# Kernel tuning notes

Hardware: AMD Instinct MI355X
Metric: run time of the kernel (lower is better)

The kernel has to match this reference:

```python
import jax, jax.numpy as jnp
import numpy as np

N = 50000      # nodes
E = 800000     # edges (avg degree 16)
F_IN = 64      # node_feature_space
H = 64         # hidden_dim
G = 16         # graphs in batch
BN_EPS = 1e-5


def setup_inputs() -> dict:
    key = jax.random.key(0)
    ks = jax.random.split(key, 8)
    x = jax.random.normal(ks[0], (N, F_IN), jnp.float32)
    edge_index = jax.random.randint(ks[1], (2, E), 0, N, dtype=jnp.int64)
    batch = jnp.sort(jax.random.randint(ks[2], (N,), 0, G, dtype=jnp.int64))
    init = lambda k, shp, fan: jax.random.normal(k, shp, jnp.float32) / np.float32(np.sqrt(fan))
    params = dict(
        W1_0=init(ks[3], (F_IN, H), F_IN), b1_0=jnp.zeros((H,), jnp.float32),
        W2_0=init(ks[4], (H, H), H),       b2_0=jnp.zeros((H,), jnp.float32),
        g_0=jnp.ones((H,), jnp.float32),   be_0=jnp.zeros((H,), jnp.float32),
        W1_1=init(ks[5], (H, H), H),       b1_1=jnp.zeros((H,), jnp.float32),
        W2_1=init(ks[6], (H, H), H),       b2_1=jnp.zeros((H,), jnp.float32),
        g_1=jnp.ones((H,), jnp.float32),   be_1=jnp.zeros((H,), jnp.float32),
    )
    return dict(x=x, edge_index=edge_index, batch=batch, **params)


def _gin_layer(x, src, dst, W1, b1, W2, b2, g, be):
    # GINConv (eps=0): h_i = MLP(x_i + sum_{j->i} x_j)
    agg = jax.ops.segment_sum(x[src], dst, num_segments=N)   # [N, d]
    h = x + agg
    h = jnp.maximum(h @ W1 + b1, 0.0) @ W2 + b2              # Linear-ReLU-Linear
    # BatchNorm1d (training-mode batch stats, biased variance as in torch)
    mu = h.mean(axis=0)
    var = h.var(axis=0)
    h = (h - mu) * jax.lax.rsqrt(var + BN_EPS) * g + be
    return jnp.maximum(h, 0.0)                               # ReLU


def reference(x, edge_index, batch,
              W1_0, b1_0, W2_0, b2_0, g_0, be_0,
              W1_1, b1_1, W2_1, b2_1, g_1, be_1):
    src, dst = edge_index[0], edge_index[1]
    x = _gin_layer(x, src, dst, W1_0, b1_0, W2_0, b2_0, g_0, be_0)
    x = _gin_layer(x, src, dst, W1_1, b1_1, W2_1, b2_1, g_1, be_1)
    # global_mean_pool over graph ids
    cnt = jax.ops.segment_sum(jnp.ones((N,), x.dtype), batch, num_segments=G)
    sums = jax.ops.segment_sum(x, batch, num_segments=G)
    h_graph = sums / jnp.maximum(cnt, 1.0)[:, None]
    return (x, h_graph)
```

## Files before the change

### kernel.cpp

```cpp
#include <hip/hip_runtime.h>
#include <hip/hip_bf16.h>


constexpr int NN = 50000;
constexpr int NE = 800000;
constexpr int HD = 64;
constexpr int NG = 16;
constexpr float BN_EPS = 1e-5f;
constexpr int SCAN_BLOCKS = (NN + 255) / 256;
constexpr int NBUCK = (NN + 1023) / 1024;
constexpr int BIN1_BLOCKS = (NE + 4095) / 4096;

__global__ __launch_bounds__(256)
void x2bf_kernel(const float* __restrict__ x, __hip_bfloat16* __restrict__ xb,
                 int* __restrict__ cnt) {
    int i4 = blockIdx.x * 256 + threadIdx.x;
    if (i4 < NN) cnt[i4] = 0;
    if (i4 >= NN * HD / 4) return;
    float4 v = *(const float4*)(x + (size_t)i4 * 4);
    union { ushort4 u; __hip_bfloat16 b[4]; } p;
    p.b[0] = __float2bfloat16(v.x);
    p.b[1] = __float2bfloat16(v.y);
    p.b[2] = __float2bfloat16(v.z);
    p.b[3] = __float2bfloat16(v.w);
    *(ushort4*)((unsigned short*)xb + (size_t)i4 * 4) = p.u;
}

__global__ __launch_bounds__(256)
void count_kernel(const int* __restrict__ ei, int* __restrict__ cnt) {
    int e4 = (blockIdx.x * 256 + threadIdx.x) * 4;
    if (e4 >= NE) return;
    int4 d = *(const int4*)(ei + NE + e4);
    atomicAdd(&cnt[d.x], 1);
    atomicAdd(&cnt[d.y], 1);
    atomicAdd(&cnt[d.z], 1);
    atomicAdd(&cnt[d.w], 1);
}

__global__ __launch_bounds__(256)
void scan1_kernel(const int* __restrict__ cnt, int* __restrict__ row_ptr,
                  int* __restrict__ partials) {
    int i = blockIdx.x * 256 + threadIdx.x;
    int v = (i < NN) ? cnt[i] : 0;
    __shared__ int s[256];
    s[threadIdx.x] = v;
    __syncthreads();
#pragma unroll
    for (int off = 1; off < 256; off <<= 1) {
        int add = (threadIdx.x >= off) ? s[threadIdx.x - off] : 0;
        __syncthreads();
        s[threadIdx.x] += add;
        __syncthreads();
    }
    if (i < NN) row_ptr[i] = s[threadIdx.x] - v;
    if (threadIdx.x == 255) partials[blockIdx.x] = s[255];
}

__global__ __launch_bounds__(256)
void scan3_kernel(int* __restrict__ row_ptr, const int* __restrict__ partials,
                  int* __restrict__ gcur) {
    __shared__ int s[256];
    __shared__ int orig[256];
    int v = (threadIdx.x < SCAN_BLOCKS) ? partials[threadIdx.x] : 0;
    s[threadIdx.x] = v;
    orig[threadIdx.x] = v;
    __syncthreads();
#pragma unroll
    for (int off = 1; off < 256; off <<= 1) {
        int add = (threadIdx.x >= off) ? s[threadIdx.x - off] : 0;
        __syncthreads();
        s[threadIdx.x] += add;
        __syncthreads();
    }
    int poff = s[blockIdx.x] - orig[blockIdx.x];
    int i = blockIdx.x * 256 + threadIdx.x;
    if (i < NN) {
        int rv = row_ptr[i] + poff;
        row_ptr[i] = rv;
        if ((i & 1023) == 0) gcur[i >> 10] = rv;
    }
    if (i == 0) row_ptr[NN] = NE;
}

__global__ __launch_bounds__(256)
void bin1_kernel(const int* __restrict__ ei, int* __restrict__ gcur,
                 int2* __restrict__ part) {
    __shared__ int lcnt[NBUCK];
    __shared__ int lbase[NBUCK];
    __shared__ int lcur[NBUCK];
    int tid = threadIdx.x;
    int chunk = blockIdx.x * 4096;
    if (tid < NBUCK) lcnt[tid] = 0;
    __syncthreads();
#pragma unroll
    for (int r = 0; r < 16; r++) {
        int e = chunk + r * 256 + tid;
        if (e < NE) atomicAdd(&lcnt[ei[NE + e] >> 10], 1);
    }
    __syncthreads();
    if (tid < NBUCK) {
        lbase[tid] = atomicAdd(&gcur[tid], lcnt[tid]);
        lcur[tid] = 0;
    }
    __syncthreads();
#pragma unroll
    for (int r = 0; r < 16; r++) {
        int e = chunk + r * 256 + tid;
        if (e < NE) {
            int src = ei[e];
            int dst = ei[NE + e];
            int b = dst >> 10;
            int slot = atomicAdd(&lcur[b], 1);
            part[lbase[b] + slot] = make_int2(src, dst);
        }
    }
}

__global__ __launch_bounds__(256)
void bin2_kernel(const int2* __restrict__ part, const int* __restrict__ row_ptr,
                 int* __restrict__ csr) {
    __shared__ int lcur[1024];
    int b = blockIdx.x;
    int base_row = b << 10;
    for (int i = threadIdx.x; i < 1024; i += 256)
        lcur[i] = row_ptr[min(base_row + i, NN)];
    __syncthreads();
    int s = row_ptr[min(base_row, NN)];
    int e = row_ptr[min(base_row + 1024, NN)];
    for (int i = s + threadIdx.x; i < e; i += 256) {
        int2 p = part[i];
        int pos = atomicAdd(&lcur[p.y & 1023], 1);
        csr[pos] = p.x;
    }
}

__global__ __launch_bounds__(256)
void agg_kernel(const float* __restrict__ x, const __hip_bfloat16* __restrict__ xb,
                const int* __restrict__ row_ptr, const int* __restrict__ csr,
                float* __restrict__ h, float* __restrict__ stats) {
    if (blockIdx.x == 0 && threadIdx.x < 128) stats[threadIdx.x] = 0.f;
    int row = blockIdx.x * 4 + (threadIdx.x >> 6);
    int lane = threadIdx.x & 63;
    int s = row_ptr[row], e = row_ptr[row + 1];
    int cnt = e - s;
    int ids = (lane < cnt) ? csr[s + lane] : 0;
    float acc = x[(size_t)row * HD + lane];
    int m = min(cnt, 64);
    int j = 0;
    float a0 = 0.f, a1 = 0.f, a2 = 0.f, a3 = 0.f;
    float a4 = 0.f, a5 = 0.f, a6 = 0.f, a7 = 0.f;
    for (; j + 8 <= m; j += 8) {
        int nb0 = __shfl(ids, j);
        int nb1 = __shfl(ids, j + 1);
        int nb2 = __shfl(ids, j + 2);
        int nb3 = __shfl(ids, j + 3);
        int nb4 = __shfl(ids, j + 4);
        int nb5 = __shfl(ids, j + 5);
        int nb6 = __shfl(ids, j + 6);
        int nb7 = __shfl(ids, j + 7);
        a0 += __bfloat162float(xb[(size_t)nb0 * HD + lane]);
        a1 += __bfloat162float(xb[(size_t)nb1 * HD + lane]);
        a2 += __bfloat162float(xb[(size_t)nb2 * HD + lane]);
        a3 += __bfloat162float(xb[(size_t)nb3 * HD + lane]);
        a4 += __bfloat162float(xb[(size_t)nb4 * HD + lane]);
        a5 += __bfloat162float(xb[(size_t)nb5 * HD + lane]);
        a6 += __bfloat162float(xb[(size_t)nb6 * HD + lane]);
        a7 += __bfloat162float(xb[(size_t)nb7 * HD + lane]);
    }
    acc += ((a0 + a1) + (a2 + a3)) + ((a4 + a5) + (a6 + a7));
    for (; j < m; j++) {
        int nb = __shfl(ids, j);
        acc += __bfloat162float(xb[(size_t)nb * HD + lane]);
    }
    for (int jj = s + 64; jj < e; jj++) {
        acc += __bfloat162float(xb[(size_t)csr[jj] * HD + lane]);
    }
    h[(size_t)row * HD + lane] = acc;
}

__global__ __launch_bounds__(256)
void aggn_kernel(const float* __restrict__ hraw, const __hip_bfloat16* __restrict__ xbr,
                 const int* __restrict__ row_ptr, const int* __restrict__ csr,
                 const float* __restrict__ stats_prev, const float* __restrict__ g0,
                 const float* __restrict__ be0,
                 float* __restrict__ h, float* __restrict__ stats_next) {
    if (blockIdx.x == 0 && threadIdx.x < 128) stats_next[threadIdx.x] = 0.f;
    int row = blockIdx.x * 4 + (threadIdx.x >> 6);
    int lane = threadIdx.x & 63;
    const float inv = 1.f / (float)NN;
    float mu = stats_prev[lane] * inv;
    float var = stats_prev[64 + lane] * inv - mu * mu;
    float sc = g0[lane] * rsqrtf(var + BN_EPS);
    float off = be0[lane] - mu * sc;
    int s = row_ptr[row], e = row_ptr[row + 1];
    int cnt = e - s;
    int ids = (lane < cnt) ? csr[s + lane] : 0;
    float acc = fmaxf(fmaf(hraw[(size_t)row * HD + lane], sc, off), 0.f);
    int m = min(cnt, 64);
    int j = 0;
    float a0 = 0.f, a1 = 0.f, a2 = 0.f, a3 = 0.f;
    float a4 = 0.f, a5 = 0.f, a6 = 0.f, a7 = 0.f;
    for (; j + 8 <= m; j += 8) {
        int nb0 = __shfl(ids, j);
        int nb1 = __shfl(ids, j + 1);
        int nb2 = __shfl(ids, j + 2);
        int nb3 = __shfl(ids, j + 3);
        int nb4 = __shfl(ids, j + 4);
        int nb5 = __shfl(ids, j + 5);
        int nb6 = __shfl(ids, j + 6);
        int nb7 = __shfl(ids, j + 7);
        float v0 = __bfloat162float(xbr[(size_t)nb0 * HD + lane]);
        float v1 = __bfloat162float(xbr[(size_t)nb1 * HD + lane]);
        float v2 = __bfloat162float(xbr[(size_t)nb2 * HD + lane]);
        float v3 = __bfloat162float(xbr[(size_t)nb3 * HD + lane]);
        float v4 = __bfloat162float(xbr[(size_t)nb4 * HD + lane]);
        float v5 = __bfloat162float(xbr[(size_t)nb5 * HD + lane]);
        float v6 = __bfloat162float(xbr[(size_t)nb6 * HD + lane]);
        float v7 = __bfloat162float(xbr[(size_t)nb7 * HD + lane]);
        a0 += fmaxf(fmaf(v0, sc, off), 0.f);
        a1 += fmaxf(fmaf(v1, sc, off), 0.f);
        a2 += fmaxf(fmaf(v2, sc, off), 0.f);
        a3 += fmaxf(fmaf(v3, sc, off), 0.f);
        a4 += fmaxf(fmaf(v4, sc, off), 0.f);
        a5 += fmaxf(fmaf(v5, sc, off), 0.f);
        a6 += fmaxf(fmaf(v6, sc, off), 0.f);
        a7 += fmaxf(fmaf(v7, sc, off), 0.f);
    }
    acc += ((a0 + a1) + (a2 + a3)) + ((a4 + a5) + (a6 + a7));
    for (; j < m; j++) {
        int nb = __shfl(ids, j);
        float v = __bfloat162float(xbr[(size_t)nb * HD + lane]);
        acc += fmaxf(fmaf(v, sc, off), 0.f);
    }
    for (int jj = s + 64; jj < e; jj++) {
        float v = __bfloat162float(xbr[(size_t)csr[jj] * HD + lane]);
        acc += fmaxf(fmaf(v, sc, off), 0.f);
    }
    h[(size_t)row * HD + lane] = acc;
}

__global__ __launch_bounds__(256)
void mlp_kernel(const float* __restrict__ hin, float* __restrict__ hout,
                const float* __restrict__ W1, const float* __restrict__ b1,
                const float* __restrict__ W2, const float* __restrict__ b2,
                float* __restrict__ stats, float* __restrict__ psums,
                __hip_bfloat16* __restrict__ xbr) {
    __shared__ float sh[128 * 65];
    __shared__ float sW[64 * 64];
    __shared__ float sb[64];
    __shared__ float red[2][4][64];
    int tid = threadIdx.x;
    int base = blockIdx.x * 128;

    if (blockIdx.x == 0) {
        float4 z = make_float4(0.f, 0.f, 0.f, 0.f);
        *(float4*)(psums + tid * 4) = z;
    }
    for (int i = tid; i < 4096; i += 256) sW[i] = W1[i];
    if (tid < 64) sb[tid] = b1[tid];
#pragma unroll
    for (int i = 0; i < 8; i++) {
        int i4 = tid + 256 * i;
        int row = i4 >> 4, col = (i4 & 15) * 4;
        int grow = base + row;
        float4 v = (grow < NN) ? *(const float4*)(hin + (size_t)grow * HD + col)
                               : make_float4(0.f, 0.f, 0.f, 0.f);
        float* d = sh + row * 65 + col;
        d[0] = v.x; d[1] = v.y; d[2] = v.z; d[3] = v.w;
    }
    __syncthreads();

    int wv = tid >> 6;
    int lane = tid & 63;

    float acc0[16], acc1[16];
#pragma unroll
    for (int j = 0; j < 16; j++) { acc0[j] = sb[wv * 16 + j]; acc1[j] = acc0[j]; }
    for (int k = 0; k < 64; k++) {
        float a0 = sh[lane * 65 + k];
        float a1 = sh[(64 + lane) * 65 + k];
        const float4* wr = (const float4*)(sW + k * 64 + wv * 16);
#pragma unroll
        for (int q = 0; q < 4; q++) {
            float4 w = wr[q];
            acc0[4 * q + 0] = fmaf(a0, w.x, acc0[4 * q + 0]);
            acc0[4 * q + 1] = fmaf(a0, w.y, acc0[4 * q + 1]);
            acc0[4 * q + 2] = fmaf(a0, w.z, acc0[4 * q + 2]);
            acc0[4 * q + 3] = fmaf(a0, w.w, acc0[4 * q + 3]);
            acc1[4 * q + 0] = fmaf(a1, w.x, acc1[4 * q + 0]);
            acc1[4 * q + 1] = fmaf(a1, w.y, acc1[4 * q + 1]);
            acc1[4 * q + 2] = fmaf(a1, w.z, acc1[4 * q + 2]);
            acc1[4 * q + 3] = fmaf(a1, w.w, acc1[4 * q + 3]);
        }
    }
    __syncthreads();

#pragma unroll
    for (int j = 0; j < 16; j++) {
        sh[lane * 65 + wv * 16 + j] = fmaxf(acc0[j], 0.f);
        sh[(64 + lane) * 65 + wv * 16 + j] = fmaxf(acc1[j], 0.f);
    }
    for (int i = tid; i < 4096; i += 256) sW[i] = W2[i];
    if (tid < 64) sb[tid] = b2[tid];
    __syncthreads();

#pragma unroll
    for (int j = 0; j < 16; j++) { acc0[j] = sb[wv * 16 + j]; acc1[j] = acc0[j]; }
    for (int k = 0; k < 64; k++) {
        float a0 = sh[lane * 65 + k];
        float a1 = sh[(64 + lane) * 65 + k];
        const float4* wr = (const float4*)(sW + k * 64 + wv * 16);
#pragma unroll
        for (int q = 0; q < 4; q++) {
            float4 w = wr[q];
            acc0[4 * q + 0] = fmaf(a0, w.x, acc0[4 * q + 0]);
            acc0[4 * q + 1] = fmaf(a0, w.y, acc0[4 * q + 1]);
            acc0[4 * q + 2] = fmaf(a0, w.z, acc0[4 * q + 2]);
            acc0[4 * q + 3] = fmaf(a0, w.w, acc0[4 * q + 3]);
            acc1[4 * q + 0] = fmaf(a1, w.x, acc1[4 * q + 0]);
            acc1[4 * q + 1] = fmaf(a1, w.y, acc1[4 * q + 1]);
            acc1[4 * q + 2] = fmaf(a1, w.z, acc1[4 * q + 2]);
            acc1[4 * q + 3] = fmaf(a1, w.w, acc1[4 * q + 3]);
        }
    }
    __syncthreads();
#pragma unroll
    for (int j = 0; j < 16; j++) {
        sh[lane * 65 + wv * 16 + j] = acc0[j];
        sh[(64 + lane) * 65 + wv * 16 + j] = acc1[j];
    }
    __syncthreads();

#pragma unroll
    for (int i = 0; i < 8; i++) {
        int i4 = tid + 256 * i;
        int row = i4 >> 4, col = (i4 & 15) * 4;
        int grow = base + row;
        if (grow < NN) {
            const float* s = sh + row * 65 + col;
            float4 v = make_float4(s[0], s[1], s[2], s[3]);
            *(float4*)(hout + (size_t)grow * HD + col) = v;
            if (xbr) {
                union { ushort4 u; __hip_bfloat16 b[4]; } p;
                p.b[0] = __float2bfloat16(v.x);
                p.b[1] = __float2bfloat16(v.y);
                p.b[2] = __float2bfloat16(v.z);
                p.b[3] = __float2bfloat16(v.w);
                *(ushort4*)((unsigned short*)xbr + (size_t)grow * HD + col) = p.u;
            }
        }
    }

    {
        int col = tid & 63;
        int r0 = (tid >> 6) * 32;
        float s = 0.f, ss = 0.f;
#pragma unroll
        for (int r = 0; r < 32; r++) {
            float v = (base + r0 + r < NN) ? sh[(r0 + r) * 65 + col] : 0.f;
            s += v;
            ss += v * v;
        }
        red[0][tid >> 6][col] = s;
        red[1][tid >> 6][col] = ss;
        __syncthreads();
        if (tid < 64) {
            float S = red[0][0][col] + red[0][1][col] + red[0][2][col] + red[0][3][col];
            atomicAdd(stats + col, S);
        } else if (tid < 128) {
            float SS = red[1][0][col] + red[1][1][col] + red[1][2][col] + red[1][3][col];
            atomicAdd(stats + 64 + col, SS);
        }
    }
}

__global__ __launch_bounds__(256)
void norm_kernel(float* h, const float* __restrict__ stats,
                 const float* __restrict__ g, const float* __restrict__ be,
                 const int* __restrict__ batch, float* __restrict__ psums) {
    __shared__ float sg[2][64];
    if (threadIdx.x < 128) sg[threadIdx.x >> 6][threadIdx.x & 63] = 0.f;
    __syncthreads();
    size_t i4 = (size_t)blockIdx.x * 256 + threadIdx.x;
    int row = (int)(i4 >> 4);
    int base_row = blockIdx.x * 16;
    int g0 = batch[base_row];
    size_t off = i4 * 4;
    int col = (int)(off & 63);
    float4 v = *(const float4*)(h + off);
    float4 sm = *(const float4*)(stats + col);
    float4 sq = *(const float4*)(stats + 64 + col);
    float4 gg = *(const float4*)(g + col);
    float4 bb = *(const float4*)(be + col);
    const float inv = 1.f / (float)NN;
    float4 o;
    {
        float mu = sm.x * inv, var = sq.x * inv - mu * mu;
        float sc = gg.x * rsqrtf(var + BN_EPS);
        o.x = fmaxf((v.x - mu) * sc + bb.x, 0.f);
    }
    {
        float mu = sm.y * inv, var = sq.y * inv - mu * mu;
        float sc = gg.y * rsqrtf(var + BN_EPS);
        o.y = fmaxf((v.y - mu) * sc + bb.y, 0.f);
    }
    {
        float mu = sm.z * inv, var = sq.z * inv - mu * mu;
        float sc = gg.z * rsqrtf(var + BN_EPS);
        o.z = fmaxf((v.z - mu) * sc + bb.z, 0.f);
    }
    {
        float mu = sm.w * inv, var = sq.w * inv - mu * mu;
        float sc = gg.w * rsqrtf(var + BN_EPS);
        o.w = fmaxf((v.w - mu) * sc + bb.w, 0.f);
    }
    *(float4*)(h + off) = o;

    int dg = batch[row] - g0;
    if (dg <= 1) {
        atomicAdd(&sg[dg][col + 0], o.x);
        atomicAdd(&sg[dg][col + 1], o.y);
        atomicAdd(&sg[dg][col + 2], o.z);
        atomicAdd(&sg[dg][col + 3], o.w);
    } else {
        int gid = g0 + dg;
        atomicAdd(&psums[gid * HD + col + 0], o.x);
        atomicAdd(&psums[gid * HD + col + 1], o.y);
        atomicAdd(&psums[gid * HD + col + 2], o.z);
        atomicAdd(&psums[gid * HD + col + 3], o.w);
    }
    __syncthreads();
    if (threadIdx.x < 128) {
        int d = threadIdx.x >> 6;
        int c = threadIdx.x & 63;
        float s = sg[d][c];
        if (g0 + d < NG && s != 0.f) atomicAdd(&psums[(g0 + d) * HD + c], s);
    }
}

__device__ __forceinline__ int lower_bound_batch(const int* __restrict__ b, int val) {
    int lo = 0, hi = NN;
    while (lo < hi) {
        int mid = (lo + hi) >> 1;
        if (b[mid] < val) lo = mid + 1;
        else hi = mid;
    }
    return lo;
}

__global__ __launch_bounds__(1024)
void pool_finalize_kernel(const float* __restrict__ sums, const int* __restrict__ batch,
                          float* __restrict__ out) {
    int g = threadIdx.x >> 6;
    int col = threadIdx.x & 63;
    int s = lower_bound_batch(batch, g);
    int e = lower_bound_batch(batch, g + 1);
    float cnt = (float)(e - s);
    out[g * HD + col] = sums[g * HD + col] / fmaxf(cnt, 1.f);
}

extern "C" void kernel_launch(void* const* d_in, const int* in_sizes, int n_in,
                              void* d_out, int out_size, void* d_ws, size_t ws_size,
                              hipStream_t stream) {
    const float* x = (const float*)d_in[0];
    const int* ei = (const int*)d_in[1];
    const int* batch = (const int*)d_in[2];
    const float* W1_0 = (const float*)d_in[3];
    const float* b1_0 = (const float*)d_in[4];
    const float* W2_0 = (const float*)d_in[5];
    const float* b2_0 = (const float*)d_in[6];
    const float* g_0 = (const float*)d_in[7];
    const float* be_0 = (const float*)d_in[8];
    const float* W1_1 = (const float*)d_in[9];
    const float* b1_1 = (const float*)d_in[10];
    const float* W2_1 = (const float*)d_in[11];
    const float* b2_1 = (const float*)d_in[12];
    const float* g_1 = (const float*)d_in[13];
    const float* be_1 = (const float*)d_in[14];

    float* out = (float*)d_out;

    float* buf_h = (float*)d_ws;
    float* stats0 = buf_h + (size_t)NN * HD;
    float* stats1 = stats0 + 128;
    float* psums = stats1 + 128;
    int* row_ptr = (int*)(psums + 1024);
    int* cnt = row_ptr + (NN + 2);
    int* partials = cnt + NN;
    int* gcur = partials + 256;
    int* csr = gcur + 64;
    __hip_bfloat16* xb = (__hip_bfloat16*)(csr + NE);
    int2* part = (int2*)(xb + (size_t)NN * HD);

    dim3 b256(256);
    int mlp_grid = (NN + 127) / 128;
    int norm_grid = (NN * HD / 4 + 255) / 256;
    int cnt_grid = (NE / 4 + 255) / 256;
    int agg_grid = NN / 4;

    x2bf_kernel<<<norm_grid, b256, 0, stream>>>(x, xb, cnt);
    count_kernel<<<cnt_grid, b256, 0, stream>>>(ei, cnt);
    scan1_kernel<<<SCAN_BLOCKS, b256, 0, stream>>>(cnt, row_ptr, partials);
    scan3_kernel<<<SCAN_BLOCKS, b256, 0, stream>>>(row_ptr, partials, gcur);
    bin1_kernel<<<BIN1_BLOCKS, b256, 0, stream>>>(ei, gcur, part);
    bin2_kernel<<<NBUCK, b256, 0, stream>>>(part, row_ptr, csr);

    agg_kernel<<<agg_grid, b256, 0, stream>>>(x, xb, row_ptr, csr, buf_h, stats0);
    mlp_kernel<<<mlp_grid, b256, 0, stream>>>(buf_h, out, W1_0, b1_0, W2_0, b2_0,
                                              stats0, psums, xb);

    aggn_kernel<<<agg_grid, b256, 0, stream>>>(out, xb, row_ptr, csr,
                                               stats0, g_0, be_0, buf_h, stats1);
    mlp_kernel<<<mlp_grid, b256, 0, stream>>>(buf_h, out, W1_1, b1_1, W2_1, b2_1,
                                              stats1, psums, (__hip_bfloat16*)nullptr);

    norm_kernel<<<norm_grid, b256, 0, stream>>>(out, stats1, g_1, be_1, batch, psums);
    pool_finalize_kernel<<<1, dim3(1024), 0, stream>>>(psums, batch, out + (size_t)NN * HD);
}
```

Before: 322.2 us.

## Merge scan passes with decoupled lookback and fold pooling finalize into norm

```diff
diff --git a/kernel.cpp b/kernel.cpp
--- a/kernel.cpp
+++ b/kernel.cpp
@@ -13,9 +13,10 @@
 
 __global__ __launch_bounds__(256)
 void x2bf_kernel(const float* __restrict__ x, __hip_bfloat16* __restrict__ xb,
-                 int* __restrict__ cnt) {
+                 int* __restrict__ cnt, int* __restrict__ flags) {
     int i4 = blockIdx.x * 256 + threadIdx.x;
     if (i4 < NN) cnt[i4] = 0;
+    if (i4 < 256) flags[i4] = 0;
     if (i4 >= NN * HD / 4) return;
     float4 v = *(const float4*)(x + (size_t)i4 * 4);
     union { ushort4 u; __hip_bfloat16 b[4]; } p;
@@ -38,11 +39,13 @@
 }
 
 __global__ __launch_bounds__(256)
-void scan1_kernel(const int* __restrict__ cnt, int* __restrict__ row_ptr,
-                  int* __restrict__ partials) {
-    int i = blockIdx.x * 256 + threadIdx.x;
+void scan_kernel(const int* __restrict__ cnt, int* __restrict__ row_ptr,
+                 int* __restrict__ flags, int* __restrict__ gcur) {
+    int b = blockIdx.x;
+    int i = b * 256 + threadIdx.x;
     int v = (i < NN) ? cnt[i] : 0;
     __shared__ int s[256];
+    __shared__ int pre[256];
     s[threadIdx.x] = v;
     __syncthreads();
 #pragma unroll
@@ -52,30 +55,23 @@
         s[threadIdx.x] += add;
         __syncthreads();
     }
-    if (i < NN) row_ptr[i] = s[threadIdx.x] - v;
-    if (threadIdx.x == 255) partials[blockIdx.x] = s[255];
-}
-
-__global__ __launch_bounds__(256)
-void scan3_kernel(int* __restrict__ row_ptr, const int* __restrict__ partials,
-                  int* __restrict__ gcur) {
-    __shared__ int s[256];
-    __shared__ int orig[256];
-    int v = (threadIdx.x < SCAN_BLOCKS) ? partials[threadIdx.x] : 0;
-    s[threadIdx.x] = v;
-    orig[threadIdx.x] = v;
-    __syncthreads();
-#pragma unroll
-    for (int off = 1; off < 256; off <<= 1) {
-        int add = (threadIdx.x >= off) ? s[threadIdx.x - off] : 0;
+    if (threadIdx.x == 255) atomicExch(&flags[b], s[255] | 0x40000000);
+    int pv = 0;
+    if (threadIdx.x < b) {
+        int f;
+        do { f = atomicAdd(&flags[threadIdx.x], 0); } while (f == 0);
+        pv = f & 0x3FFFFFFF;
+    }
+    pre[threadIdx.x] = pv;
+    __syncthreads();
+#pragma unroll
+    for (int off = 128; off > 0; off >>= 1) {
+        if (threadIdx.x < off) pre[threadIdx.x] += pre[threadIdx.x + off];
         __syncthreads();
-        s[threadIdx.x] += add;
-        __syncthreads();
-    }
-    int poff = s[blockIdx.x] - orig[blockIdx.x];
-    int i = blockIdx.x * 256 + threadIdx.x;
+    }
+    int poff = pre[0];
     if (i < NN) {
-        int rv = row_ptr[i] + poff;
+        int rv = s[threadIdx.x] - v + poff;
         row_ptr[i] = rv;
         if ((i & 1023) == 0) gcur[i >> 10] = rv;
     }
@@ -243,7 +239,7 @@
 void mlp_kernel(const float* __restrict__ hin, float* __restrict__ hout,
                 const float* __restrict__ W1, const float* __restrict__ b1,
                 const float* __restrict__ W2, const float* __restrict__ b2,
-                float* __restrict__ stats, float* __restrict__ psums,
+                float* __restrict__ stats, float* __restrict__ gout,
                 __hip_bfloat16* __restrict__ xbr) {
     __shared__ float sh[128 * 65];
     __shared__ float sW[64 * 64];
@@ -254,7 +250,7 @@
 
     if (blockIdx.x == 0) {
         float4 z = make_float4(0.f, 0.f, 0.f, 0.f);
-        *(float4*)(psums + tid * 4) = z;
+        *(float4*)(gout + tid * 4) = z;
     }
     for (int i = tid; i < 4096; i += 256) sW[i] = W1[i];
     if (tid < 64) sb[tid] = b1[tid];
@@ -374,17 +370,40 @@
     }
 }
 
+__device__ __forceinline__ int lower_bound_batch(const int* __restrict__ b, int val) {
+    int lo = 0, hi = NN;
+    while (lo < hi) {
+        int mid = (lo + hi) >> 1;
+        if (b[mid] < val) lo = mid + 1;
+        else hi = mid;
+    }
+    return lo;
+}
+
 __global__ __launch_bounds__(256)
 void norm_kernel(float* h, const float* __restrict__ stats,
                  const float* __restrict__ g, const float* __restrict__ be,
-                 const int* __restrict__ batch, float* __restrict__ psums) {
+                 const int* __restrict__ batch, float* __restrict__ gout) {
     __shared__ float sg[2][64];
-    if (threadIdx.x < 128) sg[threadIdx.x >> 6][threadIdx.x & 63] = 0.f;
-    __syncthreads();
-    size_t i4 = (size_t)blockIdx.x * 256 + threadIdx.x;
-    int row = (int)(i4 >> 4);
+    __shared__ float rinv[2];
+    int tid = threadIdx.x;
+    if (tid < 128) sg[tid >> 6][tid & 63] = 0.f;
     int base_row = blockIdx.x * 16;
     int g0 = batch[base_row];
+    if (tid < 2) {
+        int gg = g0 + tid;
+        float r = 0.f;
+        if (gg < NG) {
+            int s = lower_bound_batch(batch, gg);
+            int e = lower_bound_batch(batch, gg + 1);
+            r = 1.f / fmaxf((float)(e - s), 1.f);
+        }
+        rinv[tid] = r;
+    }
+    __syncthreads();
+
+    size_t i4 = (size_t)blockIdx.x * 256 + tid;
+    int row = (int)(i4 >> 4);
     size_t off = i4 * 4;
     int col = (int)(off & 63);
     float4 v = *(const float4*)(h + off);
@@ -424,39 +443,22 @@
         atomicAdd(&sg[dg][col + 3], o.w);
     } else {
         int gid = g0 + dg;
-        atomicAdd(&psums[gid * HD + col + 0], o.x);
-        atomicAdd(&psums[gid * HD + col + 1], o.y);
-        atomicAdd(&psums[gid * HD + col + 2], o.z);
-        atomicAdd(&psums[gid * HD + col + 3], o.w);
-    }
-    __syncthreads();
-    if (threadIdx.x < 128) {
-        int d = threadIdx.x >> 6;
-        int c = threadIdx.x & 63;
+        int s = lower_bound_batch(batch, gid);
+        int e = lower_bound_batch(batch, gid + 1);
+        float r = 1.f / fmaxf((float)(e - s), 1.f);
+        atomicAdd(&gout[gid * HD + col + 0], o.x * r);
+        atomicAdd(&gout[gid * HD + col + 1], o.y * r);
+        atomicAdd(&gout[gid * HD + col + 2], o.z * r);
+        atomicAdd(&gout[gid * HD + col + 3], o.w * r);
+    }
+    __syncthreads();
+    if (tid < 128) {
+        int d = tid >> 6;
+        int c = tid & 63;
         float s = sg[d][c];
-        if (g0 + d < NG && s != 0.f) atomicAdd(&psums[(g0 + d) * HD + c], s);
-    }
-}
-
-__device__ __forceinline__ int lower_bound_batch(const int* __restrict__ b, int val) {
-    int lo = 0, hi = NN;
-    while (lo < hi) {
-        int mid = (lo + hi) >> 1;
-        if (b[mid] < val) lo = mid + 1;
-        else hi = mid;
-    }
-    return lo;
-}
-
-__global__ __launch_bounds__(1024)
-void pool_finalize_kernel(const float* __restrict__ sums, const int* __restrict__ batch,
-                          float* __restrict__ out) {
-    int g = threadIdx.x >> 6;
-    int col = threadIdx.x & 63;
-    int s = lower_bound_batch(batch, g);
-    int e = lower_bound_batch(batch, g + 1);
-    float cnt = (float)(e - s);
-    out[g * HD + col] = sums[g * HD + col] / fmaxf(cnt, 1.f);
+        if (g0 + d < NG && s != 0.f)
+            atomicAdd(&gout[(g0 + d) * HD + c], s * rinv[d]);
+    }
 }
 
 extern "C" void kernel_launch(void* const* d_in, const int* in_sizes, int n_in,
@@ -479,15 +481,15 @@
     const float* be_1 = (const float*)d_in[14];
 
     float* out = (float*)d_out;
+    float* gout = out + (size_t)NN * HD;
 
     float* buf_h = (float*)d_ws;
     float* stats0 = buf_h + (size_t)NN * HD;
     float* stats1 = stats0 + 128;
-    float* psums = stats1 + 128;
-    int* row_ptr = (int*)(psums + 1024);
+    int* flags = (int*)(stats1 + 128);
+    int* row_ptr = flags + 256;
     int* cnt = row_ptr + (NN + 2);
-    int* partials = cnt + NN;
-    int* gcur = partials + 256;
+    int* gcur = cnt + NN;
     int* csr = gcur + 64;
     __hip_bfloat16* xb = (__hip_bfloat16*)(csr + NE);
     int2* part = (int2*)(xb + (size_t)NN * HD);
@@ -498,22 +500,20 @@
     int cnt_grid = (NE / 4 + 255) / 256;
     int agg_grid = NN / 4;
 
-    x2bf_kernel<<<norm_grid, b256, 0, stream>>>(x, xb, cnt);
+    x2bf_kernel<<<norm_grid, b256, 0, stream>>>(x, xb, cnt, flags);
     count_kernel<<<cnt_grid, b256, 0, stream>>>(ei, cnt);
-    scan1_kernel<<<SCAN_BLOCKS, b256, 0, stream>>>(cnt, row_ptr, partials);
-    scan3_kernel<<<SCAN_BLOCKS, b256, 0, stream>>>(row_ptr, partials, gcur);
+    scan_kernel<<<SCAN_BLOCKS, b256, 0, stream>>>(cnt, row_ptr, flags, gcur);
     bin1_kernel<<<BIN1_BLOCKS, b256, 0, stream>>>(ei, gcur, part);
     bin2_kernel<<<NBUCK, b256, 0, stream>>>(part, row_ptr, csr);
 
     agg_kernel<<<agg_grid, b256, 0, stream>>>(x, xb, row_ptr, csr, buf_h, stats0);
     mlp_kernel<<<mlp_grid, b256, 0, stream>>>(buf_h, out, W1_0, b1_0, W2_0, b2_0,
-                                              stats0, psums, xb);
+                                              stats0, gout, xb);
 
     aggn_kernel<<<agg_grid, b256, 0, stream>>>(out, xb, row_ptr, csr,
                                                stats0, g_0, be_0, buf_h, stats1);
     mlp_kernel<<<mlp_grid, b256, 0, stream>>>(buf_h, out, W1_1, b1_1, W2_1, b2_1,
-                                              stats1, psums, (__hip_bfloat16*)nullptr);
-
-    norm_kernel<<<norm_grid, b256, 0, stream>>>(out, stats1, g_1, be_1, batch, psums);
-    pool_finalize_kernel<<<1, dim3(1024), 0, stream>>>(psums, batch, out + (size_t)NN * HD);
-}
+                                              stats1, gout, (__hip_bfloat16*)nullptr);
+
+    norm_kernel<<<norm_grid, b256, 0, stream>>>(out, stats1, g_1, be_1, batch, gout);
+}
```

Result: no change. 323.2 us (+0.3%).
